# Kernel optimization log

Measured on AMD Instinct MI355X. Metric: run time of the kernel, lower is better.

## Reference

```python
import jax, jax.numpy as jnp
import numpy as np


def setup_inputs() -> dict:
    key = jax.random.key(0)
    kX, kA, kB, kC = jax.random.split(key, 4)
    Bsz, L, H, P, S = 2, 4096, 16, 64, 64
    X = jax.random.normal(kX, (Bsz, L, H, P), jnp.float32)
    # log-space negative decay per head (docstring: 'scalar decay per head (log space, negative)')
    A = -0.1 * jax.random.uniform(kA, (Bsz, L, H), jnp.float32)
    Bm = jax.random.normal(kB, (Bsz, L, H, S), jnp.float32) / np.sqrt(S).astype(np.float32)
    Cm = jax.random.normal(kC, (Bsz, L, H, S), jnp.float32) / np.sqrt(S).astype(np.float32)
    return {"X": X, "A": A, "B": Bm, "C": Cm, "chunk_size": 64}


def _ssd_forward(X, A, B, C, chunk_size):
    batch, seqlen, H, P = X.shape
    S = B.shape[-1]
    cs = chunk_size
    orig_seqlen = seqlen
    pad = (-seqlen) % cs
    if pad:
        X = jnp.pad(X, ((0, 0), (0, pad), (0, 0), (0, 0)))
        A = jnp.pad(A, ((0, 0), (0, pad), (0, 0)))
        B = jnp.pad(B, ((0, 0), (0, pad), (0, 0), (0, 0)))
        C = jnp.pad(C, ((0, 0), (0, pad), (0, 0), (0, 0)))
        seqlen = seqlen + pad
    n = seqlen // cs
    # reshape to chunks and move heads forward: [b, h, n, c, ...]
    Xc = X.reshape(batch, n, cs, H, P).transpose(0, 3, 1, 2, 4)
    Ac = A.reshape(batch, n, cs, H).transpose(0, 3, 1, 2)          # [b,h,n,c]
    Bc = B.reshape(batch, n, cs, H, S).transpose(0, 3, 1, 2, 4)
    Cc = C.reshape(batch, n, cs, H, S).transpose(0, 3, 1, 2, 4)
    Acs = jnp.cumsum(Ac, axis=-1)                                   # [b,h,n,c]
    # causal decay matrix L: exp(A_i - A_j) for i>=j; masked entries get -inf
    # then clamp(-inf, -100, 100) -> -100, exp(-100) ~ 3.7e-44 (faithful to torch order)
    diff = Acs[..., :, None] - Acs[..., None, :]                    # [b,h,n,c,c]
    causal = jnp.arange(cs)[:, None] >= jnp.arange(cs)[None, :]
    log_diff = jnp.clip(jnp.where(causal, diff, -jnp.inf), -100.0, 100.0)
    Lmat = jnp.nan_to_num(jnp.exp(log_diff), nan=0.0, posinf=1.0, neginf=0.0)
    # intra-chunk (attention-like) term
    CB = jnp.einsum('bhnis,bhnjs->bhnij', Cc, Bc)
    Y_intra = jnp.einsum('bhnij,bhnjp->bhnip', Lmat * CB, Xc)
    # inter-chunk state recurrence
    decay_chunk = jnp.exp(jnp.sum(Ac, axis=-1))                     # [b,h,n]
    decay_to_end = jnp.exp(Acs[..., -1:] - Acs)                     # [b,h,n,c]
    h_final = jnp.einsum('bhnc,bhncs,bhncp->bhnsp', decay_to_end, Bc, Xc)
    def step(carry, xs):
        d, hf = xs
        new_carry = d[..., None, None] * carry + hf
        return new_carry, carry  # h_inter[c] is state BEFORE chunk c
    d_scan = jnp.moveaxis(decay_chunk, 2, 0)                        # [n,b,h]
    h_scan = jnp.moveaxis(h_final, 2, 0)                            # [n,b,h,s,p]
    init = jnp.zeros((batch, H, S, P), X.dtype)
    _, h_inter = jax.lax.scan(step, init, (d_scan, h_scan))
    h_inter = jnp.moveaxis(h_inter, 0, 2)                           # [b,h,n,s,p]
    decay_from_start = jnp.exp(Acs)
    Y_inter = jnp.einsum('bhnis,bhnsp,bhni->bhnip', Cc, h_inter, decay_from_start)
    Y = (Y_intra + Y_inter).transpose(0, 2, 3, 1, 4).reshape(batch, seqlen, H, P)
    return Y[:, :orig_seqlen]


def reference(X, A, B, C, chunk_size):
    return _ssd_forward(X, A, B, C, chunk_size)
```

## Files before the change

kernel.cpp:

```cpp
#include <hip/hip_runtime.h>


#define BSZ 2
#define LSEQ 4096
#define NH 16
#define NC 64
#define NCH (BSZ * NH * NC)
#define SCAN_G 8
#define CHW 4096
#define TILE_USHORTS ((size_t)NCH * CHW)

typedef float f32x4 __attribute__((ext_vector_type(4)));
typedef __bf16 bf16x8 __attribute__((ext_vector_type(8)));

union FragU { uint4 u; bf16x8 b; };

__device__ __forceinline__ unsigned short f2b(float x) {
    union { float f; unsigned u; } c; c.f = x;
    unsigned r = c.u + 0x7fffu + ((c.u >> 16) & 1u);
    return (unsigned short)(r >> 16);
}
__device__ __forceinline__ float b2f(unsigned short v) {
    union { unsigned u; float f; } c; c.u = ((unsigned)v) << 16;
    return c.f;
}

__device__ __forceinline__ int rm_e(int row, int k) { return row * 64 + (k ^ ((row & 7) << 3)); }
__device__ __forceinline__ int tr_e(int row, int k) { return row * 64 + (k ^ (((row >> 1) & 7) << 3)); }

__device__ __forceinline__ bf16x8 frag_rm(const unsigned short* buf, int tile, int kk, int l) {
    FragU f; f.u = *(const uint4*)&buf[rm_e(tile * 16 + (l & 15), kk * 32 + ((l >> 4) << 3))];
    return f.b;
}
__device__ __forceinline__ bf16x8 frag_tr(const unsigned short* buf, int tile, int kk, int l) {
    FragU f; f.u = *(const uint4*)&buf[tr_e(tile * 16 + (l & 15), kk * 32 + ((l >> 4) << 3))];
    return f.b;
}

__global__ __launch_bounds__(256) void ssd_k1(
    const float* __restrict__ Xg, const float* __restrict__ Ag,
    const float* __restrict__ Bg, const float* __restrict__ Cg,
    unsigned short* __restrict__ hws, unsigned short* __restrict__ Mws,
    unsigned short* __restrict__ Csws, float* __restrict__ dws)
{
    __shared__ __align__(16) unsigned short sBrm[64 * 64];
    __shared__ __align__(16) unsigned short sCrm[64 * 64];
    __shared__ __align__(16) unsigned short sBt[64 * 64];
    __shared__ __align__(16) unsigned short sXt[64 * 64];
    __shared__ float sE[64], sR[64], sDte[64];

    const int tid = threadIdx.x;
    const int l = tid & 63;
    const int w = tid >> 6;
    const int n = blockIdx.x & (NC - 1);
    const int h = (blockIdx.x >> 6) & (NH - 1);
    const int b = blockIdx.x >> 10;
    const int row0 = b * LSEQ + n * 64;
    const unsigned chb = (unsigned)blockIdx.x * CHW;

    float4 xv[4], bv[4], cv[4];
    const int p0 = (tid & 15) * 4;
    #pragma unroll
    for (int it = 0; it < 4; ++it) {
        const int c = (tid >> 4) + it * 16;
        const unsigned g = ((unsigned)(row0 + c) * NH + h) * 64 + p0;
        xv[it] = *(const float4*)&Xg[g];
        bv[it] = *(const float4*)&Bg[g];
        cv[it] = *(const float4*)&Cg[g];
    }
    if (tid < 64) {
        float a = Ag[(unsigned)(row0 + tid) * NH + h];
        #pragma unroll
        for (int off = 1; off < 64; off <<= 1) {
            float v = __shfl_up(a, off, 64);
            if (tid >= off) a += v;
        }
        const float a63 = __shfl(a, 63, 64);
        sE[tid] = __expf(a);
        sR[tid] = __expf(-a);
        sDte[tid] = __expf(a63 - a);
        if (tid == 63) dws[blockIdx.x] = __expf(a63);
    }
    __syncthreads();

    #pragma unroll
    for (int it = 0; it < 4; ++it) {
        const int c = (tid >> 4) + it * 16;
        const float dte = sDte[c];
        const float Ec = sE[c];
        ushort4 bw; bw.x = f2b(bv[it].x); bw.y = f2b(bv[it].y); bw.z = f2b(bv[it].z); bw.w = f2b(bv[it].w);
        ushort4 cw; cw.x = f2b(cv[it].x); cw.y = f2b(cv[it].y); cw.z = f2b(cv[it].z); cw.w = f2b(cv[it].w);
        *(ushort4*)&sBrm[rm_e(c, p0)] = bw;
        *(ushort4*)&sCrm[rm_e(c, p0)] = cw;
        sBt[tr_e(p0 + 0, c)] = bw.x;
        sBt[tr_e(p0 + 1, c)] = bw.y;
        sBt[tr_e(p0 + 2, c)] = bw.z;
        sBt[tr_e(p0 + 3, c)] = bw.w;
        sXt[tr_e(p0 + 0, c)] = f2b(xv[it].x * dte);
        sXt[tr_e(p0 + 1, c)] = f2b(xv[it].y * dte);
        sXt[tr_e(p0 + 2, c)] = f2b(xv[it].z * dte);
        sXt[tr_e(p0 + 3, c)] = f2b(xv[it].w * dte);
        ushort4 sw; sw.x = f2b(cv[it].x * Ec); sw.y = f2b(cv[it].y * Ec);
        sw.z = f2b(cv[it].z * Ec); sw.w = f2b(cv[it].w * Ec);
        *(ushort4*)&Csws[chb + rm_e(c, p0)] = sw;
    }
    __syncthreads();

    const f32x4 zero = {0.f, 0.f, 0.f, 0.f};
    f32x4 accT[4] = {zero, zero, zero, zero};
    f32x4 accH[4] = {zero, zero, zero, zero};
    #pragma unroll
    for (int kk = 0; kk < 2; ++kk) {
        const bf16x8 aB = frag_rm(sBrm, w, kk, l);
        const bf16x8 aBt = frag_tr(sBt, w, kk, l);
        #pragma unroll
        for (int t = 0; t < 4; ++t) {
            accT[t] = __builtin_amdgcn_mfma_f32_16x16x32_bf16(aB, frag_rm(sCrm, t, kk, l), accT[t], 0, 0, 0);
            accH[t] = __builtin_amdgcn_mfma_f32_16x16x32_bf16(aBt, frag_tr(sXt, t, kk, l), accH[t], 0, 0, 0);
        }
    }

    const int il = (l >> 4) << 2;
    const int j0 = w * 16 + il;
    float Rj[4];
    #pragma unroll
    for (int r = 0; r < 4; ++r) Rj[r] = sR[j0 + r];
    #pragma unroll
    for (int ti = 0; ti < 4; ++ti) {
        const int i = ti * 16 + (l & 15);
        const float Ei = sE[i];
        ushort4 m;
        m.x = (i >= j0 + 0) ? f2b(Ei * Rj[0] * accT[ti][0]) : (unsigned short)0;
        m.y = (i >= j0 + 1) ? f2b(Ei * Rj[1] * accT[ti][1]) : (unsigned short)0;
        m.z = (i >= j0 + 2) ? f2b(Ei * Rj[2] * accT[ti][2]) : (unsigned short)0;
        m.w = (i >= j0 + 3) ? f2b(Ei * Rj[3] * accT[ti][3]) : (unsigned short)0;
        *(ushort4*)&Mws[chb + rm_e(i, j0)] = m;
    }
    const int s0 = w * 16 + il;
    #pragma unroll
    for (int tp = 0; tp < 4; ++tp) {
        const int p = tp * 16 + (l & 15);
        ushort4 o;
        o.x = f2b(accH[tp][0]); o.y = f2b(accH[tp][1]);
        o.z = f2b(accH[tp][2]); o.w = f2b(accH[tp][3]);
        *(ushort4*)&hws[chb + rm_e(p, s0)] = o;
    }
}

__global__ __launch_bounds__(256) void ssd_scan(unsigned short* __restrict__ hws,
                                                const float* __restrict__ dws)
{
    __shared__ float sD[NC];
    const int tid = threadIdx.x;
    const int bh = blockIdx.x / SCAN_G;
    const int g = blockIdx.x % SCAN_G;
    if (tid < NC) sD[tid] = dws[bh * NC + tid];
    __syncthreads();

    unsigned* hw32 = (unsigned*)hws;
    const unsigned base = (unsigned)bh * NC * 2048u + g * 256u + tid;
    float cx = 0.f, cy = 0.f;
    unsigned cur = hw32[base];
    #pragma unroll 4
    for (int c = 0; c < NC; ++c) {
        unsigned nxt = 0;
        if (c < NC - 1) nxt = hw32[base + (c + 1) * 2048u];
        const float hx = b2f((unsigned short)(cur & 0xffffu));
        const float hy = b2f((unsigned short)(cur >> 16));
        hw32[base + c * 2048u] = (unsigned)f2b(cx) | ((unsigned)f2b(cy) << 16);
        const float d = sD[c];
        cx = d * cx + hx;
        cy = d * cy + hy;
        cur = nxt;
    }
}

__global__ __launch_bounds__(256) void ssd_k3(
    const float* __restrict__ Xg, const unsigned short* __restrict__ Mws,
    const unsigned short* __restrict__ Csws, const unsigned short* __restrict__ hws,
    float* __restrict__ Yg)
{
    const int tid = threadIdx.x;
    const int l = tid & 63;
    const int w = tid >> 6;
    const int n = blockIdx.x & (NC - 1);
    const int h = (blockIdx.x >> 6) & (NH - 1);
    const int b = blockIdx.x >> 10;
    const int row0 = b * LSEQ + n * 64;
    const unsigned chb = (unsigned)blockIdx.x * CHW;

    const int p = w * 16 + (l & 15);
    bf16x8 aX[2], aH[2];
    #pragma unroll
    for (int kk = 0; kk < 2; ++kk) {
        const int c0 = kk * 32 + ((l >> 4) << 3);
        bf16x8 x;
        #pragma unroll
        for (int e = 0; e < 8; ++e)
            x[e] = (__bf16)Xg[((unsigned)(row0 + c0 + e) * NH + h) * 64 + p];
        aX[kk] = x;
        FragU f; f.u = *(const uint4*)&hws[chb + rm_e(p, c0)];
        aH[kk] = f.b;
    }

    const f32x4 zero = {0.f, 0.f, 0.f, 0.f};
    f32x4 accY[4] = {zero, zero, zero, zero};
    f32x4 accI[4] = {zero, zero, zero, zero};
    #pragma unroll
    for (int kk = 0; kk < 2; ++kk) {
        #pragma unroll
        for (int ti = 0; ti < 4; ++ti) {
            const int ke = kk * 32 + ((l >> 4) << 3);
            const int ic = ti * 16 + (l & 15);
            FragU mf; mf.u = *(const uint4*)&Mws[chb + rm_e(ic, ke)];
            FragU cf; cf.u = *(const uint4*)&Csws[chb + rm_e(ic, ke)];
            accY[ti] = __builtin_amdgcn_mfma_f32_16x16x32_bf16(aX[kk], mf.b, accY[ti], 0, 0, 0);
            accI[ti] = __builtin_amdgcn_mfma_f32_16x16x32_bf16(aH[kk], cf.b, accI[ti], 0, 0, 0);
        }
    }

    const int il = (l >> 4) << 2;
    const int pbase = w * 16 + il;
    #pragma unroll
    for (int ti = 0; ti < 4; ++ti) {
        const int i = ti * 16 + (l & 15);
        float4 o;
        o.x = accY[ti][0] + accI[ti][0];
        o.y = accY[ti][1] + accI[ti][1];
        o.z = accY[ti][2] + accI[ti][2];
        o.w = accY[ti][3] + accI[ti][3];
        *(float4*)&Yg[((unsigned)(row0 + i) * NH + h) * 64 + pbase] = o;
    }
}

extern "C" void kernel_launch(void* const* d_in, const int* in_sizes, int n_in,
                              void* d_out, int out_size, void* d_ws, size_t ws_size,
                              hipStream_t stream) {
    const float* X = (const float*)d_in[0];
    const float* A = (const float*)d_in[1];
    const float* Bm = (const float*)d_in[2];
    const float* Cm = (const float*)d_in[3];
    float* Y = (float*)d_out;
    unsigned short* hws = (unsigned short*)d_ws;
    unsigned short* Mws = hws + TILE_USHORTS;
    unsigned short* Csws = Mws + TILE_USHORTS;
    float* dws = (float*)(Csws + TILE_USHORTS);

    ssd_k1<<<NCH, 256, 0, stream>>>(X, A, Bm, Cm, hws, Mws, Csws, dws);
    ssd_scan<<<BSZ * NH * SCAN_G, 256, 0, stream>>>(hws, dws);
    ssd_k3<<<NCH, 256, 0, stream>>>(X, Mws, Csws, hws, Y);
}
```

Before: 66.83 us.

## Replace sequential chunk-state scan with MFMA matmul over decay weights

The sequential scan over 64 chunks (256 blocks, one serial loop each) becomes a parallel kernel with 2048 blocks. Each block builds a lower-triangular decay-weight matrix from prefix sums of the per-chunk log decays and applies it to the chunk states with bf16 MFMA. The workspace layouts for M, C-scaled and h are also changed to a fragment-ordered layout so k3 loads are contiguous. This trades a latency-bound serial loop for extra matmul work and extra bf16 rounding of the weights.

```diff
diff --git a/kernel.cpp b/kernel.cpp
--- a/kernel.cpp
+++ b/kernel.cpp
@@ -6,23 +6,18 @@
 #define NH 16
 #define NC 64
 #define NCH (BSZ * NH * NC)
-#define SCAN_G 8
 #define CHW 4096
 #define TILE_USHORTS ((size_t)NCH * CHW)
 
 typedef float f32x4 __attribute__((ext_vector_type(4)));
 typedef __bf16 bf16x8 __attribute__((ext_vector_type(8)));
 
-union FragU { uint4 u; bf16x8 b; };
+union FragU { uint4 u; bf16x8 b; unsigned short s[8]; };
 
 __device__ __forceinline__ unsigned short f2b(float x) {
     union { float f; unsigned u; } c; c.f = x;
     unsigned r = c.u + 0x7fffu + ((c.u >> 16) & 1u);
     return (unsigned short)(r >> 16);
-}
-__device__ __forceinline__ float b2f(unsigned short v) {
-    union { unsigned u; float f; } c; c.u = ((unsigned)v) << 16;
-    return c.f;
 }
 
 __device__ __forceinline__ int rm_e(int row, int k) { return row * 64 + (k ^ ((row & 7) << 3)); }
@@ -79,7 +74,7 @@
         sE[tid] = __expf(a);
         sR[tid] = __expf(-a);
         sDte[tid] = __expf(a63 - a);
-        if (tid == 63) dws[blockIdx.x] = __expf(a63);
+        if (tid == 63) dws[blockIdx.x] = a63;
     }
     __syncthreads();
 
@@ -100,9 +95,15 @@
         sXt[tr_e(p0 + 1, c)] = f2b(xv[it].y * dte);
         sXt[tr_e(p0 + 2, c)] = f2b(xv[it].z * dte);
         sXt[tr_e(p0 + 3, c)] = f2b(xv[it].w * dte);
-        ushort4 sw; sw.x = f2b(cv[it].x * Ec); sw.y = f2b(cv[it].y * Ec);
-        sw.z = f2b(cv[it].z * Ec); sw.w = f2b(cv[it].w * Ec);
-        *(ushort4*)&Csws[chb + rm_e(c, p0)] = sw;
+        {
+            const int kk = p0 >> 5;
+            const int ti0 = c >> 4;
+            const int lt = ((p0 >> 3) & 3) * 16 + (c & 15);
+            const int e0 = p0 & 7;
+            ushort4 sw; sw.x = f2b(cv[it].x * Ec); sw.y = f2b(cv[it].y * Ec);
+            sw.z = f2b(cv[it].z * Ec); sw.w = f2b(cv[it].w * Ec);
+            *(ushort4*)&Csws[chb + (((kk * 4 + ti0) * 64 + lt) << 3) + e0] = sw;
+        }
     }
     __syncthreads();
 
@@ -134,44 +135,113 @@
         m.y = (i >= j0 + 1) ? f2b(Ei * Rj[1] * accT[ti][1]) : (unsigned short)0;
         m.z = (i >= j0 + 2) ? f2b(Ei * Rj[2] * accT[ti][2]) : (unsigned short)0;
         m.w = (i >= j0 + 3) ? f2b(Ei * Rj[3] * accT[ti][3]) : (unsigned short)0;
-        *(ushort4*)&Mws[chb + rm_e(i, j0)] = m;
-    }
-    const int s0 = w * 16 + il;
-    #pragma unroll
-    for (int tp = 0; tp < 4; ++tp) {
-        const int p = tp * 16 + (l & 15);
-        ushort4 o;
-        o.x = f2b(accH[tp][0]); o.y = f2b(accH[tp][1]);
-        o.z = f2b(accH[tp][2]); o.w = f2b(accH[tp][3]);
-        *(ushort4*)&hws[chb + rm_e(p, s0)] = o;
-    }
-}
-
-__global__ __launch_bounds__(256) void ssd_scan(unsigned short* __restrict__ hws,
-                                                const float* __restrict__ dws)
+        *(ushort4*)&Mws[chb + (((ti * 4 + w) * 64 + l) << 2)] = m;
+    }
+    {
+        const int kk = w >> 1;
+        const int q3 = ((w & 1) << 1) | (il >> 3);
+        const int e0 = il & 7;
+        const int lt = q3 * 16 + (l & 15);
+        #pragma unroll
+        for (int tp = 0; tp < 4; ++tp) {
+            ushort4 o;
+            o.x = f2b(accH[tp][0]); o.y = f2b(accH[tp][1]);
+            o.z = f2b(accH[tp][2]); o.w = f2b(accH[tp][3]);
+            *(ushort4*)&hws[chb + (((kk * 4 + tp) * 64 + lt) << 3) + e0] = o;
+        }
+    }
+}
+
+__global__ __launch_bounds__(256) void ssd_k2(
+    unsigned short* __restrict__ hws, const float* __restrict__ dws)
 {
-    __shared__ float sD[NC];
+    __shared__ __align__(16) unsigned short sHt[64 * 64];
+    __shared__ __align__(16) unsigned short sW[64 * 64];
+    __shared__ __align__(16) unsigned short sOut[64 * 64];
+    __shared__ float sI[64];
+
     const int tid = threadIdx.x;
-    const int bh = blockIdx.x / SCAN_G;
-    const int g = blockIdx.x % SCAN_G;
-    if (tid < NC) sD[tid] = dws[bh * NC + tid];
-    __syncthreads();
-
-    unsigned* hw32 = (unsigned*)hws;
-    const unsigned base = (unsigned)bh * NC * 2048u + g * 256u + tid;
-    float cx = 0.f, cy = 0.f;
-    unsigned cur = hw32[base];
-    #pragma unroll 4
-    for (int c = 0; c < NC; ++c) {
-        unsigned nxt = 0;
-        if (c < NC - 1) nxt = hw32[base + (c + 1) * 2048u];
-        const float hx = b2f((unsigned short)(cur & 0xffffu));
-        const float hy = b2f((unsigned short)(cur >> 16));
-        hw32[base + c * 2048u] = (unsigned)f2b(cx) | ((unsigned)f2b(cy) << 16);
-        const float d = sD[c];
-        cx = d * cx + hx;
-        cy = d * cy + hy;
-        cur = nxt;
+    const int l = tid & 63;
+    const int w = tid >> 6;
+    const int bh = blockIdx.x >> 6;
+    const int p = blockIdx.x & 63;
+    const int tp = p >> 4, p15 = p & 15;
+
+    const int cq = tid >> 2;
+    const int sseg = (tid & 3) << 4;
+    const unsigned fragoff =
+        (unsigned)(((((sseg >> 5) * 4 + tp) * 64 + ((sseg >> 3) & 3) * 16 + p15)) << 3);
+    const unsigned chbL = ((unsigned)(bh * 64 + cq)) * CHW;
+    const uint4 u0 = *(const uint4*)&hws[chbL + fragoff];
+    const uint4 u1 = *(const uint4*)&hws[chbL + fragoff + 128];
+
+    if (tid < 64) {
+        float a = dws[bh * 64 + tid];
+        #pragma unroll
+        for (int off = 1; off < 64; off <<= 1) {
+            float v = __shfl_up(a, off, 64);
+            if (tid >= off) a += v;
+        }
+        sI[tid] = a;
+    }
+    __syncthreads();
+
+    {
+        const int c = tid >> 2;
+        const int cb = (tid & 3) << 4;
+        const float Ic1 = (c > 0) ? sI[c - 1] : 0.f;
+        #pragma unroll
+        for (int g = 0; g < 4; ++g) {
+            ushort4 wv;
+            const int c2 = cb + g * 4;
+            wv.x = (c > c2 + 0) ? f2b(__expf(Ic1 - sI[c2 + 0])) : (unsigned short)0;
+            wv.y = (c > c2 + 1) ? f2b(__expf(Ic1 - sI[c2 + 1])) : (unsigned short)0;
+            wv.z = (c > c2 + 2) ? f2b(__expf(Ic1 - sI[c2 + 2])) : (unsigned short)0;
+            wv.w = (c > c2 + 3) ? f2b(__expf(Ic1 - sI[c2 + 3])) : (unsigned short)0;
+            *(ushort4*)&sW[rm_e(c, c2)] = wv;
+        }
+    }
+    {
+        const unsigned short* a0 = (const unsigned short*)&u0;
+        const unsigned short* a1 = (const unsigned short*)&u1;
+        #pragma unroll
+        for (int e = 0; e < 8; ++e) {
+            sHt[tr_e(sseg + e, cq)] = a0[e];
+            sHt[tr_e(sseg + 8 + e, cq)] = a1[e];
+        }
+    }
+    __syncthreads();
+
+    const f32x4 zero = {0.f, 0.f, 0.f, 0.f};
+    f32x4 acc[4] = {zero, zero, zero, zero};
+    #pragma unroll
+    for (int kk = 0; kk < 2; ++kk) {
+        const bf16x8 aH = frag_tr(sHt, w, kk, l);
+        #pragma unroll
+        for (int ti = 0; ti < 4; ++ti)
+            acc[ti] = __builtin_amdgcn_mfma_f32_16x16x32_bf16(aH, frag_rm(sW, ti, kk, l), acc[ti], 0, 0, 0);
+    }
+    const int il = (l >> 4) << 2;
+    #pragma unroll
+    for (int ti = 0; ti < 4; ++ti) {
+        const int c = ti * 16 + (l & 15);
+        #pragma unroll
+        for (int r = 0; r < 4; ++r) {
+            const int s = w * 16 + il + r;
+            sOut[s * 64 + (c ^ ((s & 7) << 3))] = f2b(acc[ti][r]);
+        }
+    }
+    __syncthreads();
+    {
+        FragU o0, o1;
+        #pragma unroll
+        for (int e = 0; e < 8; ++e) {
+            const int s0 = sseg + e, s1 = sseg + 8 + e;
+            o0.s[e] = sOut[s0 * 64 + (cq ^ ((s0 & 7) << 3))];
+            o1.s[e] = sOut[s1 * 64 + (cq ^ ((s1 & 7) << 3))];
+        }
+        *(uint4*)&hws[chbL + fragoff] = o0.u;
+        *(uint4*)&hws[chbL + fragoff + 128] = o1.u;
     }
 }
 
@@ -188,8 +258,9 @@
     const int b = blockIdx.x >> 10;
     const int row0 = b * LSEQ + n * 64;
     const unsigned chb = (unsigned)blockIdx.x * CHW;
-
-    const int p = w * 16 + (l & 15);
+    const int i15 = l & 15;
+    const int p = w * 16 + i15;
+
     bf16x8 aX[2], aH[2];
     #pragma unroll
     for (int kk = 0; kk < 2; ++kk) {
@@ -199,7 +270,7 @@
         for (int e = 0; e < 8; ++e)
             x[e] = (__bf16)Xg[((unsigned)(row0 + c0 + e) * NH + h) * 64 + p];
         aX[kk] = x;
-        FragU f; f.u = *(const uint4*)&hws[chb + rm_e(p, c0)];
+        FragU f; f.u = *(const uint4*)&hws[chb + (((kk * 4 + w) * 64 + l) << 3)];
         aH[kk] = f.b;
     }
 
@@ -208,22 +279,24 @@
     f32x4 accI[4] = {zero, zero, zero, zero};
     #pragma unroll
     for (int kk = 0; kk < 2; ++kk) {
+        const int j0 = kk * 32 + ((l >> 4) << 3);
+        const int wj = j0 >> 4;
+        const int q = (j0 >> 2) & 3;
         #pragma unroll
         for (int ti = 0; ti < 4; ++ti) {
-            const int ke = kk * 32 + ((l >> 4) << 3);
-            const int ic = ti * 16 + (l & 15);
-            FragU mf; mf.u = *(const uint4*)&Mws[chb + rm_e(ic, ke)];
-            FragU cf; cf.u = *(const uint4*)&Csws[chb + rm_e(ic, ke)];
+            FragU mf, cf;
+            *(ushort4*)&mf.s[0] = *(const ushort4*)&Mws[chb + (((ti * 4 + wj) * 64 + q * 16 + i15) << 2)];
+            *(ushort4*)&mf.s[4] = *(const ushort4*)&Mws[chb + (((ti * 4 + wj) * 64 + (q + 1) * 16 + i15) << 2)];
+            cf.u = *(const uint4*)&Csws[chb + (((kk * 4 + ti) * 64 + l) << 3)];
             accY[ti] = __builtin_amdgcn_mfma_f32_16x16x32_bf16(aX[kk], mf.b, accY[ti], 0, 0, 0);
             accI[ti] = __builtin_amdgcn_mfma_f32_16x16x32_bf16(aH[kk], cf.b, accI[ti], 0, 0, 0);
         }
     }
 
-    const int il = (l >> 4) << 2;
-    const int pbase = w * 16 + il;
+    const int pbase = w * 16 + ((l >> 4) << 2);
     #pragma unroll
     for (int ti = 0; ti < 4; ++ti) {
-        const int i = ti * 16 + (l & 15);
+        const int i = ti * 16 + i15;
         float4 o;
         o.x = accY[ti][0] + accI[ti][0];
         o.y = accY[ti][1] + accI[ti][1];
@@ -247,6 +320,6 @@
     float* dws = (float*)(Csws + TILE_USHORTS);
 
     ssd_k1<<<NCH, 256, 0, stream>>>(X, A, Bm, Cm, hws, Mws, Csws, dws);
-    ssd_scan<<<BSZ * NH * SCAN_G, 256, 0, stream>>>(hws, dws);
+    ssd_k2<<<NCH, 256, 0, stream>>>(hws, dws);
     ssd_k3<<<NCH, 256, 0, stream>>>(X, Mws, Csws, hws, Y);
 }
```

Result: slower. 84.29 us (+26.1%).

## Store workspace tiles in MFMA fragment order and prefetch deeper in scan

Applied to the files above, without the earlier changes.

The intermediate M, C-scaled and h workspace tiles are now written in the exact per-lane MFMA fragment order, so the consumer kernel reads contiguous 16-byte or 8-byte chunks per lane instead of swizzled row-major addresses. The scan kernel keeps four chunk loads in flight instead of one, to hide global memory latency along the serial recurrence. The exp of the chunk decay moves from the producer into the scan. Together these aim to make global accesses coalesced and to cut latency stalls, at the cost of more complex index arithmetic and the h layout now being shared across three kernels.

```diff
diff --git a/kernel.cpp b/kernel.cpp
--- a/kernel.cpp
+++ b/kernel.cpp
@@ -13,7 +13,7 @@
 typedef float f32x4 __attribute__((ext_vector_type(4)));
 typedef __bf16 bf16x8 __attribute__((ext_vector_type(8)));
 
-union FragU { uint4 u; bf16x8 b; };
+union FragU { uint4 u; bf16x8 b; unsigned short s[8]; };
 
 __device__ __forceinline__ unsigned short f2b(float x) {
     union { float f; unsigned u; } c; c.f = x;
@@ -79,7 +79,7 @@
         sE[tid] = __expf(a);
         sR[tid] = __expf(-a);
         sDte[tid] = __expf(a63 - a);
-        if (tid == 63) dws[blockIdx.x] = __expf(a63);
+        if (tid == 63) dws[blockIdx.x] = a63;
     }
     __syncthreads();
 
@@ -100,9 +100,15 @@
         sXt[tr_e(p0 + 1, c)] = f2b(xv[it].y * dte);
         sXt[tr_e(p0 + 2, c)] = f2b(xv[it].z * dte);
         sXt[tr_e(p0 + 3, c)] = f2b(xv[it].w * dte);
-        ushort4 sw; sw.x = f2b(cv[it].x * Ec); sw.y = f2b(cv[it].y * Ec);
-        sw.z = f2b(cv[it].z * Ec); sw.w = f2b(cv[it].w * Ec);
-        *(ushort4*)&Csws[chb + rm_e(c, p0)] = sw;
+        {
+            const int kk = p0 >> 5;
+            const int ti0 = c >> 4;
+            const int lt = ((p0 >> 3) & 3) * 16 + (c & 15);
+            const int e0 = p0 & 7;
+            ushort4 sw; sw.x = f2b(cv[it].x * Ec); sw.y = f2b(cv[it].y * Ec);
+            sw.z = f2b(cv[it].z * Ec); sw.w = f2b(cv[it].w * Ec);
+            *(ushort4*)&Csws[chb + (((kk * 4 + ti0) * 64 + lt) << 3) + e0] = sw;
+        }
     }
     __syncthreads();
 
@@ -134,16 +140,20 @@
         m.y = (i >= j0 + 1) ? f2b(Ei * Rj[1] * accT[ti][1]) : (unsigned short)0;
         m.z = (i >= j0 + 2) ? f2b(Ei * Rj[2] * accT[ti][2]) : (unsigned short)0;
         m.w = (i >= j0 + 3) ? f2b(Ei * Rj[3] * accT[ti][3]) : (unsigned short)0;
-        *(ushort4*)&Mws[chb + rm_e(i, j0)] = m;
-    }
-    const int s0 = w * 16 + il;
-    #pragma unroll
-    for (int tp = 0; tp < 4; ++tp) {
-        const int p = tp * 16 + (l & 15);
-        ushort4 o;
-        o.x = f2b(accH[tp][0]); o.y = f2b(accH[tp][1]);
-        o.z = f2b(accH[tp][2]); o.w = f2b(accH[tp][3]);
-        *(ushort4*)&hws[chb + rm_e(p, s0)] = o;
+        *(ushort4*)&Mws[chb + (((ti * 4 + w) * 64 + l) << 2)] = m;
+    }
+    {
+        const int kk = w >> 1;
+        const int q3 = ((w & 1) << 1) | (il >> 3);
+        const int e0 = il & 7;
+        const int lt = q3 * 16 + (l & 15);
+        #pragma unroll
+        for (int tp = 0; tp < 4; ++tp) {
+            ushort4 o;
+            o.x = f2b(accH[tp][0]); o.y = f2b(accH[tp][1]);
+            o.z = f2b(accH[tp][2]); o.w = f2b(accH[tp][3]);
+            *(ushort4*)&hws[chb + (((kk * 4 + tp) * 64 + lt) << 3) + e0] = o;
+        }
     }
 }
 
@@ -154,24 +164,25 @@
     const int tid = threadIdx.x;
     const int bh = blockIdx.x / SCAN_G;
     const int g = blockIdx.x % SCAN_G;
-    if (tid < NC) sD[tid] = dws[bh * NC + tid];
+    if (tid < NC) sD[tid] = __expf(dws[bh * NC + tid]);
     __syncthreads();
 
     unsigned* hw32 = (unsigned*)hws;
     const unsigned base = (unsigned)bh * NC * 2048u + g * 256u + tid;
+
+    unsigned buf[4];
+    #pragma unroll
+    for (int j = 0; j < 4; ++j) buf[j] = hw32[base + j * 2048u];
+
     float cx = 0.f, cy = 0.f;
-    unsigned cur = hw32[base];
     #pragma unroll 4
     for (int c = 0; c < NC; ++c) {
-        unsigned nxt = 0;
-        if (c < NC - 1) nxt = hw32[base + (c + 1) * 2048u];
-        const float hx = b2f((unsigned short)(cur & 0xffffu));
-        const float hy = b2f((unsigned short)(cur >> 16));
-        hw32[base + c * 2048u] = (unsigned)f2b(cx) | ((unsigned)f2b(cy) << 16);
+        const unsigned cur = buf[c & 3];
+        if (c + 4 < NC) buf[c & 3] = hw32[base + (unsigned)(c + 4) * 2048u];
+        hw32[base + (unsigned)c * 2048u] = (unsigned)f2b(cx) | ((unsigned)f2b(cy) << 16);
         const float d = sD[c];
-        cx = d * cx + hx;
-        cy = d * cy + hy;
-        cur = nxt;
+        cx = d * cx + b2f((unsigned short)(cur & 0xffffu));
+        cy = d * cy + b2f((unsigned short)(cur >> 16));
     }
 }
 
@@ -188,8 +199,9 @@
     const int b = blockIdx.x >> 10;
     const int row0 = b * LSEQ + n * 64;
     const unsigned chb = (unsigned)blockIdx.x * CHW;
-
-    const int p = w * 16 + (l & 15);
+    const int i15 = l & 15;
+    const int p = w * 16 + i15;
+
     bf16x8 aX[2], aH[2];
     #pragma unroll
     for (int kk = 0; kk < 2; ++kk) {
@@ -199,7 +211,7 @@
         for (int e = 0; e < 8; ++e)
             x[e] = (__bf16)Xg[((unsigned)(row0 + c0 + e) * NH + h) * 64 + p];
         aX[kk] = x;
-        FragU f; f.u = *(const uint4*)&hws[chb + rm_e(p, c0)];
+        FragU f; f.u = *(const uint4*)&hws[chb + (((kk * 4 + w) * 64 + l) << 3)];
         aH[kk] = f.b;
     }
 
@@ -208,22 +220,24 @@
     f32x4 accI[4] = {zero, zero, zero, zero};
     #pragma unroll
     for (int kk = 0; kk < 2; ++kk) {
+        const int j0 = kk * 32 + ((l >> 4) << 3);
+        const int wj = j0 >> 4;
+        const int q = (j0 >> 2) & 3;
         #pragma unroll
         for (int ti = 0; ti < 4; ++ti) {
-            const int ke = kk * 32 + ((l >> 4) << 3);
-            const int ic = ti * 16 + (l & 15);
-            FragU mf; mf.u = *(const uint4*)&Mws[chb + rm_e(ic, ke)];
-            FragU cf; cf.u = *(const uint4*)&Csws[chb + rm_e(ic, ke)];
+            FragU mf, cf;
+            *(ushort4*)&mf.s[0] = *(const ushort4*)&Mws[chb + (((ti * 4 + wj) * 64 + q * 16 + i15) << 2)];
+            *(ushort4*)&mf.s[4] = *(const ushort4*)&Mws[chb + (((ti * 4 + wj) * 64 + (q + 1) * 16 + i15) << 2)];
+            cf.u = *(const uint4*)&Csws[chb + (((kk * 4 + ti) * 64 + l) << 3)];
             accY[ti] = __builtin_amdgcn_mfma_f32_16x16x32_bf16(aX[kk], mf.b, accY[ti], 0, 0, 0);
             accI[ti] = __builtin_amdgcn_mfma_f32_16x16x32_bf16(aH[kk], cf.b, accI[ti], 0, 0, 0);
         }
     }
 
-    const int il = (l >> 4) << 2;
-    const int pbase = w * 16 + il;
+    const int pbase = w * 16 + ((l >> 4) << 2);
     #pragma unroll
     for (int ti = 0; ti < 4; ++ti) {
-        const int i = ti * 16 + (l & 15);
+        const int i = ti * 16 + i15;
         float4 o;
         o.x = accY[ti][0] + accI[ti][0];
         o.y = accY[ti][1] + accI[ti][1];
```

Result: slower. 75.21 us (+12.6%).
